# Kernel optimization log

Measured on AMD Instinct MI355X. Metric: run time of the kernel, lower is better.

Reference implementation:

```python
import jax, jax.numpy as jnp
import numpy as np

B, T, C = 2, 2048, 1024
H, D = 16, 64


def setup_inputs() -> dict:
    key = jax.random.key(0)
    k1, k2, k3 = jax.random.split(key, 3)
    x = jax.random.normal(k1, (B, T, C), dtype=jnp.float32)
    w_qkv = jax.random.normal(k2, (C, 3 * H * D), dtype=jnp.float32) * (C ** -0.5)
    w_proj = jax.random.normal(k3, (H * D, C), dtype=jnp.float32) * ((H * D) ** -0.5)
    sink_logit = jnp.zeros((H,), dtype=jnp.float32)
    return {"x": x, "w_qkv": w_qkv, "w_proj": w_proj, "sink_logit": sink_logit}


def reference(x, w_qkv, w_proj, sink_logit):
    b, t, c = x.shape
    qkv = x @ w_qkv                                  # [B,T,3HD]
    q, k, v = jnp.split(qkv, 3, axis=-1)
    # [B,H,T,D]
    q = q.reshape(b, t, H, D).transpose(0, 2, 1, 3)
    k = k.reshape(b, t, H, D).transpose(0, 2, 1, 3)
    v = v.reshape(b, t, H, D).transpose(0, 2, 1, 3)

    scale = 1.0 / jnp.sqrt(jnp.asarray(D, dtype=x.dtype))
    scores = jnp.einsum('bhqd,bhkd->bhqk', q, k) * scale   # [B,H,T,T]
    neg_inf = jnp.finfo(x.dtype).min
    causal = jnp.tril(jnp.ones((t, t), dtype=bool))
    scores = jnp.where(causal[None, None], scores, neg_inf)

    # sink column: per-head learnable logit b (added post-scale, V is zero)
    sink = jnp.broadcast_to(sink_logit.reshape(1, H, 1, 1), (b, H, t, 1)).astype(x.dtype)
    aug = jnp.concatenate([sink, scores], axis=-1)          # [B,H,T,T+1]
    attn = jax.nn.softmax(aug, axis=-1)
    # sink V is zero, so drop the sink column for the value contraction
    y = jnp.einsum('bhqk,bhkd->bhqd', attn[..., 1:], v)     # [B,H,T,D]
    y = y.transpose(0, 2, 1, 3).reshape(b, t, H * D)
    return y @ w_proj
```

## Files before the change

kernel.cpp:

```cpp
#include <hip/hip_runtime.h>
#include <hip/hip_bf16.h>
#include <stdint.h>

#define B_ 2
#define T_ 2048
#define C_ 1024
#define H_ 16
#define D_ 64

typedef __attribute__((ext_vector_type(8))) short short8;
typedef __attribute__((ext_vector_type(4))) float floatx4;

__device__ __forceinline__ float bf2f(uint16_t b) {
    return __uint_as_float(((uint32_t)b) << 16);
}
__device__ __forceinline__ uint16_t f2b(float f) {
    __hip_bfloat16 h = __float2bfloat16(f);
    return *(uint16_t*)&h;
}
__device__ __forceinline__ void glds16(const uint16_t* g, uint16_t* l) {
    __builtin_amdgcn_global_load_lds(
        (const __attribute__((address_space(1))) uint32_t*)g,
        (__attribute__((address_space(3))) uint32_t*)l, 16, 0, 0);
}

__global__ void canon_x(const float* __restrict__ in, uint16_t* __restrict__ out,
                        int n) {
    int i = (blockIdx.x * 256 + threadIdx.x) * 4;
    if (i >= n) return;
    float4 v = *(const float4*)(in + i);
    out[i + 0] = f2b(v.x);
    out[i + 1] = f2b(v.y);
    out[i + 2] = f2b(v.z);
    out[i + 3] = f2b(v.w);
}

__global__ void transpose_conv(const float* __restrict__ in, uint16_t* __restrict__ out,
                               int R, int W) {
    __shared__ uint16_t tile[32][33];
    int tx = threadIdx.x, ty = threadIdx.y;
    int c0 = blockIdx.x * 32, r0 = blockIdx.y * 32;
    #pragma unroll
    for (int i = 0; i < 32; i += 8)
        tile[ty + i][tx] = f2b(in[(size_t)(r0 + ty + i) * W + (c0 + tx)]);
    __syncthreads();
    #pragma unroll
    for (int i = 0; i < 32; i += 8)
        out[(size_t)(c0 + ty + i) * R + (r0 + tx)] = tile[tx][ty + i];
}

template <bool OUT_F32>
__global__ __launch_bounds__(256)
void gemm_bt(const uint16_t* __restrict__ A, const uint16_t* __restrict__ Bt,
             void* __restrict__ Cv, int M, int N, int K) {
    __shared__ uint16_t As[128][32];
    __shared__ uint16_t Bs[128][32];
    int tid = threadIdx.x;
    int wave = tid >> 6, lane = tid & 63;
    int quad = lane >> 4, l16 = lane & 15;
    int wr = (wave >> 1) * 64, wc = (wave & 1) * 64;
    int row0 = blockIdx.x * 128, col0 = blockIdx.y * 128;

    int srow = wave * 32 + (lane >> 2);
    int scol = (lane & 3) * 8;
    const uint16_t* gA1 = A + (size_t)(row0 + srow) * K + scol;
    const uint16_t* gA2 = A + (size_t)(row0 + srow + 16) * K + scol;
    const uint16_t* gB1 = Bt + (size_t)(col0 + srow) * K + scol;
    const uint16_t* gB2 = Bt + (size_t)(col0 + srow + 16) * K + scol;
    uint16_t* lA1 = &As[srow][scol];
    uint16_t* lA2 = &As[srow + 16][scol];
    uint16_t* lB1 = &Bs[srow][scol];
    uint16_t* lB2 = &Bs[srow + 16][scol];

    floatx4 acc[4][4];
    #pragma unroll
    for (int i = 0; i < 4; i++)
        #pragma unroll
        for (int j = 0; j < 4; j++)
            acc[i][j] = (floatx4){0.f, 0.f, 0.f, 0.f};

    for (int k0 = 0; k0 < K; k0 += 32) {
        __syncthreads();
        glds16(gA1 + k0, lA1);
        glds16(gA2 + k0, lA2);
        glds16(gB1 + k0, lB1);
        glds16(gB2 + k0, lB2);
        __syncthreads();
        short8 af[4], bf[4];
        #pragma unroll
        for (int i = 0; i < 4; i++)
            af[i] = *(const short8*)&As[wr + i * 16 + l16][quad * 8];
        #pragma unroll
        for (int j = 0; j < 4; j++)
            bf[j] = *(const short8*)&Bs[wc + j * 16 + l16][quad * 8];
        #pragma unroll
        for (int i = 0; i < 4; i++)
            #pragma unroll
            for (int j = 0; j < 4; j++)
                acc[i][j] = __builtin_amdgcn_mfma_f32_16x16x32_bf16(
                    af[i], bf[j], acc[i][j], 0, 0, 0);
    }
    #pragma unroll
    for (int i = 0; i < 4; i++) {
        #pragma unroll
        for (int j = 0; j < 4; j++) {
            int rbase = row0 + wr + i * 16 + quad * 4;
            int cg = col0 + wc + j * 16 + l16;
            #pragma unroll
            for (int r = 0; r < 4; r++) {
                if (OUT_F32)
                    ((float*)Cv)[(size_t)(rbase + r) * N + cg] = acc[i][j][r];
                else
                    ((uint16_t*)Cv)[(size_t)(rbase + r) * N + cg] = f2b(acc[i][j][r]);
            }
        }
    }
}

__global__ __launch_bounds__(256, 2)
void attn_mfma(const uint16_t* __restrict__ qkv,
               const float* __restrict__ sink,
               uint16_t* __restrict__ y) {
    __shared__ uint16_t Ks[2][64][72];
    __shared__ uint16_t Vt[2][64][72];
    __shared__ uint16_t Pl[4][32][72];

    int tid = threadIdx.x;
    int w = tid >> 6, lane = tid & 63;
    int quad = lane >> 4, l16 = lane & 15;

    int id = blockIdx.x;
    int pair = id >> 5, bh = id & 31;
    int b = bh >> 4, h = bh & 15;
    int strip = (w < 2) ? (31 - pair) : pair;
    int q0w = strip * 64 + (w & 1) * 32;
    int ktiles = 32 - pair;
    int myktiles = strip + 1;

    const uint16_t* qkv_b = qkv + (size_t)b * T_ * 3072;

    short8 qf[2][2];
    #pragma unroll
    for (int qt = 0; qt < 2; qt++) {
        int qrow = q0w + qt * 16 + l16;
        #pragma unroll
        for (int kd = 0; kd < 2; kd++) {
            uint4 raw = *(const uint4*)(qkv_b + (size_t)qrow * 3072 + h * 64 +
                                        kd * 32 + quad * 8);
            const uint16_t* rp = (const uint16_t*)&raw;
            short8 f;
            #pragma unroll
            for (int j = 0; j < 8; j++)
                f[j] = (short)f2b(bf2f(rp[j]) * 0.125f);
            qf[qt][kd] = f;
        }
    }

    float m_s[2], l_s[2];
    m_s[0] = m_s[1] = sink[h];
    l_s[0] = l_s[1] = 1.0f;
    floatx4 acc_o[2][4];
    #pragma unroll
    for (int qt = 0; qt < 2; qt++)
        #pragma unroll
        for (int dt = 0; dt < 4; dt++)
            acc_o[qt][dt] = (floatx4){0.f, 0.f, 0.f, 0.f};

    int t2 = tid >> 3;
    int dg = tid & 7;
    const uint16_t* kgp = qkv_b + 1024 + h * 64 + (size_t)(2 * t2) * 3072 + dg * 8;
    const uint16_t* vgp = kgp + 1024;
    int vcw = 2 * (t2 ^ (4 * dg));

    uint4 kr0 = *(const uint4*)(kgp);
    uint4 kr1 = *(const uint4*)(kgp + 3072);
    uint4 vr0 = *(const uint4*)(vgp);
    uint4 vr1 = *(const uint4*)(vgp + 3072);
    {
        *(uint4*)&Ks[0][2 * t2][dg * 8] = kr0;
        *(uint4*)&Ks[0][2 * t2 + 1][dg * 8] = kr1;
        const uint16_t* a0 = (const uint16_t*)&vr0;
        const uint16_t* a1 = (const uint16_t*)&vr1;
        #pragma unroll
        for (int j = 0; j < 8; j++)
            *(uint32_t*)&Vt[0][dg * 8 + j][vcw] =
                (uint32_t)a0[j] | ((uint32_t)a1[j] << 16);
    }
    if (ktiles > 1) {
        kr0 = *(const uint4*)(kgp + 64 * 3072);
        kr1 = *(const uint4*)(kgp + 64 * 3072 + 3072);
        vr0 = *(const uint4*)(vgp + 64 * 3072);
        vr1 = *(const uint4*)(vgp + 64 * 3072 + 3072);
    }
    __syncthreads();

    for (int kt = 0; kt < ktiles; kt++) {
        int cur = kt & 1;
        if (kt + 1 < ktiles) {
            *(uint4*)&Ks[cur ^ 1][2 * t2][dg * 8] = kr0;
            *(uint4*)&Ks[cur ^ 1][2 * t2 + 1][dg * 8] = kr1;
            const uint16_t* a0 = (const uint16_t*)&vr0;
            const uint16_t* a1 = (const uint16_t*)&vr1;
            #pragma unroll
            for (int j = 0; j < 8; j++)
                *(uint32_t*)&Vt[cur ^ 1][dg * 8 + j][vcw] =
                    (uint32_t)a0[j] | ((uint32_t)a1[j] << 16);
        }
        if (kt + 2 < ktiles) {
            size_t off = (size_t)(kt + 2) * 64 * 3072;
            kr0 = *(const uint4*)(kgp + off);
            kr1 = *(const uint4*)(kgp + off + 3072);
            vr0 = *(const uint4*)(vgp + off);
            vr1 = *(const uint4*)(vgp + off + 3072);
        }
        if (kt < myktiles) {
            short8 kf[4][2];
            #pragma unroll
            for (int rt = 0; rt < 4; rt++) {
                kf[rt][0] = *(const short8*)&Ks[cur][rt * 16 + l16][quad * 8];
                kf[rt][1] = *(const short8*)&Ks[cur][rt * 16 + l16][32 + quad * 8];
            }
            short8 vf[2][4];
            #pragma unroll
            for (int kb = 0; kb < 2; kb++)
                #pragma unroll
                for (int dt = 0; dt < 4; dt++) {
                    int d = dt * 16 + l16;
                    int col = 2 * (((kb * 16) + quad * 4) ^ (4 * (d >> 3)));
                    vf[kb][dt] = *(const short8*)&Vt[cur][d][col];
                }
            #pragma unroll
            for (int qt = 0; qt < 2; qt++) {
                floatx4 acc_s[4];
                #pragma unroll
                for (int rt = 0; rt < 4; rt++)
                    acc_s[rt] = (floatx4){0.f, 0.f, 0.f, 0.f};
                #pragma unroll
                for (int rt = 0; rt < 4; rt++) {
                    acc_s[rt] = __builtin_amdgcn_mfma_f32_16x16x32_bf16(
                        kf[rt][0], qf[qt][0], acc_s[rt], 0, 0, 0);
                    acc_s[rt] = __builtin_amdgcn_mfma_f32_16x16x32_bf16(
                        kf[rt][1], qf[qt][1], acc_s[rt], 0, 0, 0);
                }
                if (kt == strip) {
                    int qg = q0w + qt * 16 + l16;
                    #pragma unroll
                    for (int rt = 0; rt < 4; rt++) {
                        int kg = kt * 64 + rt * 16 + quad * 4;
                        #pragma unroll
                        for (int r = 0; r < 4; r++)
                            if (kg + r > qg) acc_s[rt][r] = -1e30f;
                    }
                }
                float mx = -1e30f;
                #pragma unroll
                for (int rt = 0; rt < 4; rt++)
                    #pragma unroll
                    for (int r = 0; r < 4; r++) mx = fmaxf(mx, acc_s[rt][r]);
                mx = fmaxf(mx, __shfl_xor(mx, 16));
                mx = fmaxf(mx, __shfl_xor(mx, 32));
                float mnew = fmaxf(m_s[qt], mx);
                float alpha = __expf(m_s[qt] - mnew);
                m_s[qt] = mnew;
                float psum = 0.f;
                #pragma unroll
                for (int rt = 0; rt < 4; rt++) {
                    float p0 = __expf(acc_s[rt][0] - mnew);
                    float p1 = __expf(acc_s[rt][1] - mnew);
                    float p2 = __expf(acc_s[rt][2] - mnew);
                    float p3 = __expf(acc_s[rt][3] - mnew);
                    psum += (p0 + p1) + (p2 + p3);
                    uint2 pk;
                    pk.x = (uint32_t)f2b(p0) | ((uint32_t)f2b(p1) << 16);
                    pk.y = (uint32_t)f2b(p2) | ((uint32_t)f2b(p3) << 16);
                    *(uint2*)&Pl[w][qt * 16 + l16][rt * 16 + quad * 4] = pk;
                }
                psum += __shfl_xor(psum, 16);
                psum += __shfl_xor(psum, 32);
                l_s[qt] = l_s[qt] * alpha + psum;
                #pragma unroll
                for (int r = 0; r < 4; r++) {
                    float ar = __shfl(alpha, (lane & 48) | (quad * 4 + r));
                    #pragma unroll
                    for (int dt = 0; dt < 4; dt++) acc_o[qt][dt][r] *= ar;
                }
                #pragma unroll
                for (int kb = 0; kb < 2; kb++) {
                    short8 pf = *(const short8*)&Pl[w][qt * 16 + l16][kb * 32 + quad * 8];
                    #pragma unroll
                    for (int dt = 0; dt < 4; dt++)
                        acc_o[qt][dt] = __builtin_amdgcn_mfma_f32_16x16x32_bf16(
                            pf, vf[kb][dt], acc_o[qt][dt], 0, 0, 0);
                }
            }
        }
        __syncthreads();
    }

    #pragma unroll
    for (int qt = 0; qt < 2; qt++) {
        #pragma unroll
        for (int r = 0; r < 4; r++) {
            float lr = __shfl(l_s[qt], (lane & 48) | (quad * 4 + r));
            float inv = 1.0f / lr;
            int qg = q0w + qt * 16 + quad * 4 + r;
            uint16_t* yp = y + (size_t)(b * T_ + qg) * 1024 + h * 64;
            #pragma unroll
            for (int dt = 0; dt < 4; dt++)
                yp[dt * 16 + l16] = f2b(acc_o[qt][dt][r] * inv);
        }
    }
}

extern "C" void kernel_launch(void* const* d_in, const int* in_sizes, int n_in,
                              void* d_out, int out_size, void* d_ws, size_t ws_size,
                              hipStream_t stream) {
    const float* x      = (const float*)d_in[0];
    const float* w_qkv  = (const float*)d_in[1];
    const float* w_proj = (const float*)d_in[2];
    const float* sink   = (const float*)d_in[3];
    float* out          = (float*)d_out;

    char* ws = (char*)d_ws;
    uint16_t* wt_qkv  = (uint16_t*)ws;
    uint16_t* wt_proj = (uint16_t*)(ws + 6291456);
    uint16_t* x_c     = (uint16_t*)(ws + 8388608);
    uint16_t* qkv     = (uint16_t*)(ws + 16777216);
    uint16_t* yb      = (uint16_t*)(ws + 41943040);

    canon_x<<<4194304 / 1024, 256, 0, stream>>>(x, x_c, 4194304);
    transpose_conv<<<dim3(3072 / 32, 1024 / 32), dim3(32, 8), 0, stream>>>(
        w_qkv, wt_qkv, 1024, 3072);
    transpose_conv<<<dim3(1024 / 32, 1024 / 32), dim3(32, 8), 0, stream>>>(
        w_proj, wt_proj, 1024, 1024);

    gemm_bt<false><<<dim3(4096 / 128, 3072 / 128), 256, 0, stream>>>(
        x_c, wt_qkv, qkv, 4096, 3072, 1024);

    attn_mfma<<<dim3(16 * 32), 256, 0, stream>>>(qkv, sink, yb);

    gemm_bt<true><<<dim3(4096 / 128, 1024 / 128), 256, 0, stream>>>(
        yb, wt_proj, out, 4096, 1024, 1024);
}
```

Baseline: 200.1 us.

## Double-buffer GEMM LDS tiles with K=64 steps, XOR swizzle, and XCD-aware block remap

Rewrites the bf16 GEMM main loop to use two LDS buffers with a K-step of 64. The next tile is loaded asynchronously with global_load_lds while MFMAs run on the current one, leaving one barrier per iteration instead of two. LDS columns are XOR-swizzled to avoid bank conflicts on the fragment reads. Blocks are launched on a 1D grid and remapped so consecutive tiles group by chiplet for L2 locality, and launch bounds now request two waves per SIMD. The risk is that the larger 64 KB LDS footprint limits occupancy.

Measured after the change: 197.8 us. Within noise of the previous version (-1.2%).

```diff
diff --git a/kernel.cpp b/kernel.cpp
--- a/kernel.cpp
+++ b/kernel.cpp
@@ -50,27 +50,29 @@
 }
 
 template <bool OUT_F32>
-__global__ __launch_bounds__(256)
+__global__ __launch_bounds__(256, 2)
 void gemm_bt(const uint16_t* __restrict__ A, const uint16_t* __restrict__ Bt,
              void* __restrict__ Cv, int M, int N, int K) {
-    __shared__ uint16_t As[128][32];
-    __shared__ uint16_t Bs[128][32];
+    __shared__ uint16_t As[2][128][64];
+    __shared__ uint16_t Bs[2][128][64];
     int tid = threadIdx.x;
-    int wave = tid >> 6, lane = tid & 63;
+    int w = tid >> 6, lane = tid & 63;
     int quad = lane >> 4, l16 = lane & 15;
-    int wr = (wave >> 1) * 64, wc = (wave & 1) * 64;
-    int row0 = blockIdx.x * 128, col0 = blockIdx.y * 128;
-
-    int srow = wave * 32 + (lane >> 2);
-    int scol = (lane & 3) * 8;
-    const uint16_t* gA1 = A + (size_t)(row0 + srow) * K + scol;
-    const uint16_t* gA2 = A + (size_t)(row0 + srow + 16) * K + scol;
-    const uint16_t* gB1 = Bt + (size_t)(col0 + srow) * K + scol;
-    const uint16_t* gB2 = Bt + (size_t)(col0 + srow + 16) * K + scol;
-    uint16_t* lA1 = &As[srow][scol];
-    uint16_t* lA2 = &As[srow + 16][scol];
-    uint16_t* lB1 = &Bs[srow][scol];
-    uint16_t* lB2 = &Bs[srow + 16][scol];
+    int wr = (w >> 1) * 64, wc = (w & 1) * 64;
+
+    int nwg = gridDim.x;
+    int wg = (blockIdx.x & 7) * (nwg >> 3) + (blockIdx.x >> 3);
+    int nby = N >> 7;
+    int row0 = (wg / nby) * 128;
+    int col0 = (wg % nby) * 128;
+
+    int sr = w * 32 + (lane >> 3);
+    int gsc = ((lane & 7) ^ (lane >> 3)) * 8;
+    uint16_t* lA = &As[0][sr][(lane & 7) * 8];
+    uint16_t* lB = &Bs[0][sr][(lane & 7) * 8];
+    const size_t LBUF = 128 * 64;
+    const uint16_t* gA = A + (size_t)(row0 + sr) * K + gsc;
+    const uint16_t* gB = Bt + (size_t)(col0 + sr) * K + gsc;
 
     floatx4 acc[4][4];
     #pragma unroll
@@ -79,27 +81,42 @@
         for (int j = 0; j < 4; j++)
             acc[i][j] = (floatx4){0.f, 0.f, 0.f, 0.f};
 
-    for (int k0 = 0; k0 < K; k0 += 32) {
+#define STAGE_(buf, k0)                                                     \
+    {                                                                       \
+        _Pragma("unroll") for (int j = 0; j < 4; j++) {                     \
+            glds16(gA + (size_t)j * 8 * K + (k0), lA + (buf)*LBUF + j * 8 * 64); \
+            glds16(gB + (size_t)j * 8 * K + (k0), lB + (buf)*LBUF + j * 8 * 64); \
+        }                                                                   \
+    }
+
+    int NT = K >> 6;
+    STAGE_(0, 0);
+    __syncthreads();
+
+    for (int t = 0; t < NT; ++t) {
+        int cur = t & 1;
+        if (t + 1 < NT) STAGE_(cur ^ 1, (t + 1) << 6);
+        #pragma unroll
+        for (int kk = 0; kk < 2; kk++) {
+            int s = ((kk * 4 + quad) ^ (l16 & 7)) * 8;
+            short8 af[4], bf[4];
+            #pragma unroll
+            for (int i = 0; i < 4; i++)
+                af[i] = *(const short8*)&As[cur][wr + i * 16 + l16][s];
+            #pragma unroll
+            for (int j = 0; j < 4; j++)
+                bf[j] = *(const short8*)&Bs[cur][wc + j * 16 + l16][s];
+            #pragma unroll
+            for (int i = 0; i < 4; i++)
+                #pragma unroll
+                for (int j = 0; j < 4; j++)
+                    acc[i][j] = __builtin_amdgcn_mfma_f32_16x16x32_bf16(
+                        af[i], bf[j], acc[i][j], 0, 0, 0);
+        }
         __syncthreads();
-        glds16(gA1 + k0, lA1);
-        glds16(gA2 + k0, lA2);
-        glds16(gB1 + k0, lB1);
-        glds16(gB2 + k0, lB2);
-        __syncthreads();
-        short8 af[4], bf[4];
-        #pragma unroll
-        for (int i = 0; i < 4; i++)
-            af[i] = *(const short8*)&As[wr + i * 16 + l16][quad * 8];
-        #pragma unroll
-        for (int j = 0; j < 4; j++)
-            bf[j] = *(const short8*)&Bs[wc + j * 16 + l16][quad * 8];
-        #pragma unroll
-        for (int i = 0; i < 4; i++)
-            #pragma unroll
-            for (int j = 0; j < 4; j++)
-                acc[i][j] = __builtin_amdgcn_mfma_f32_16x16x32_bf16(
-                    af[i], bf[j], acc[i][j], 0, 0, 0);
-    }
+    }
+#undef STAGE_
+
     #pragma unroll
     for (int i = 0; i < 4; i++) {
         #pragma unroll
@@ -334,11 +351,11 @@
     transpose_conv<<<dim3(1024 / 32, 1024 / 32), dim3(32, 8), 0, stream>>>(
         w_proj, wt_proj, 1024, 1024);
 
-    gemm_bt<false><<<dim3(4096 / 128, 3072 / 128), 256, 0, stream>>>(
+    gemm_bt<false><<<dim3(768), 256, 0, stream>>>(
         x_c, wt_qkv, qkv, 4096, 3072, 1024);
 
     attn_mfma<<<dim3(16 * 32), 256, 0, stream>>>(qkv, sink, yb);
 
-    gemm_bt<true><<<dim3(4096 / 128, 1024 / 128), 256, 0, stream>>>(
+    gemm_bt<true><<<dim3(256), 256, 0, stream>>>(
         yb, wt_proj, out, 4096, 1024, 1024);
 }
```
